# Kernel tuning notes

Hardware: AMD Instinct MI355X
Metric: run time of the kernel (lower is better)

The kernel has to match this reference:

```python
import jax, jax.numpy as jnp
import numpy as np

WS = 8   # window size
NH = 8   # num heads


def layernorm(x, g, b, eps=1e-5):
    m = jnp.mean(x, axis=-1, keepdims=True)
    v = jnp.var(x, axis=-1, keepdims=True)
    return (x - m) * jax.lax.rsqrt(v + eps) * g + b


def setup_inputs() -> dict:
    key = jax.random.key(0)
    ks = jax.random.split(key, 8)
    B, C, H, W = 16, 256, 64, 64
    s = 0.02
    inp = {
        "x": jax.random.normal(ks[0], (B, C, H, W), jnp.float32),
        "norm1_g": jnp.ones((C,), jnp.float32),
        "norm1_b": jnp.zeros((C,), jnp.float32),
        "qkv_w": jax.random.normal(ks[1], (3 * C, C), jnp.float32) * s,
        "qkv_b": jnp.zeros((3 * C,), jnp.float32),
        "rel_bias_table": jax.random.normal(ks[2], ((2 * WS - 1) ** 2, NH), jnp.float32) * s,
        "proj_w": jax.random.normal(ks[3], (C, C), jnp.float32) * s,
        "proj_b": jnp.zeros((C,), jnp.float32),
        "norm2_g": jnp.ones((C,), jnp.float32),
        "norm2_b": jnp.zeros((C,), jnp.float32),
        "fc1_w": jax.random.normal(ks[4], (4 * C, C), jnp.float32) * s,
        "fc1_b": jnp.zeros((4 * C,), jnp.float32),
        "fc2_w": jax.random.normal(ks[5], (C, 4 * C), jnp.float32) * s,
        "fc2_b": jnp.zeros((C,), jnp.float32),
    }
    # relative position index (Swin standard), shape (WS*WS, WS*WS), int constant
    coords = np.stack(np.meshgrid(np.arange(WS), np.arange(WS), indexing="ij")).reshape(2, -1)
    rel = (coords[:, :, None] - coords[:, None, :]).transpose(1, 2, 0)
    rel[:, :, 0] += WS - 1
    rel[:, :, 1] += WS - 1
    rel[:, :, 0] *= 2 * WS - 1
    inp["rel_index"] = jnp.asarray(rel.sum(-1), jnp.int32)
    return inp


def reference(x, norm1_g, norm1_b, qkv_w, qkv_b, rel_bias_table, proj_w, proj_b,
              norm2_g, norm2_b, fc1_w, fc1_b, fc2_w, fc2_b, rel_index):
    B, C, H, W = x.shape
    N = WS * WS
    hd = C // NH
    scale = hd ** -0.5

    xs = jnp.transpose(x, (0, 2, 3, 1)).reshape(B, H * W, C)  # b (h w) c
    shortcut = xs

    y = layernorm(xs, norm1_g, norm1_b).reshape(B, H, W, C)
    # window partition -> (B*nW, N, C); shift_size = 0 (default), no cyclic shift / mask
    y = y.reshape(B, H // WS, WS, W // WS, WS, C).transpose(0, 1, 3, 2, 4, 5).reshape(-1, N, C)

    qkv = (y @ qkv_w.T + qkv_b).reshape(-1, N, 3, NH, hd).transpose(2, 0, 3, 1, 4)
    q, k, v = qkv[0], qkv[1], qkv[2]  # each (nW*B, NH, N, hd)

    attn = jnp.einsum("whnd,whmd->whnm", q * scale, k)
    bias = rel_bias_table[rel_index].transpose(2, 0, 1)  # (NH, N, N)
    attn = jax.nn.softmax(attn + bias[None], axis=-1)
    out = jnp.einsum("whnm,whmd->whnd", attn, v).transpose(0, 2, 1, 3).reshape(-1, N, C)
    out = out @ proj_w.T + proj_b

    # window reverse -> (B, H*W, C)
    out = out.reshape(B, H // WS, W // WS, WS, WS, C).transpose(0, 1, 3, 2, 4, 5).reshape(B, H * W, C)

    xs = shortcut + out
    h = layernorm(xs, norm2_g, norm2_b)
    h = jax.nn.gelu(h @ fc1_w.T + fc1_b, approximate=False) @ fc2_w.T + fc2_b
    xs = xs + h

    return jnp.transpose(xs.reshape(B, H, W, C), (0, 3, 1, 2))
```

## Files before the change

### kernel.cpp

```cpp
#include <hip/hip_runtime.h>

typedef unsigned short u16;
typedef __attribute__((ext_vector_type(8))) short short8;
typedef __attribute__((ext_vector_type(4))) float f32x4;

#define MFMA16(a, b, c) __builtin_amdgcn_mfma_f32_16x16x32_bf16((a), (b), (c), 0, 0, 0)

__device__ __forceinline__ u16 f2b(float f) {
  unsigned b = __float_as_uint(f);
  b += 0x7FFFu + ((b >> 16) & 1u);
  return (u16)(b >> 16);
}

__device__ __forceinline__ void gload_lds16(const void* g, void* l) {
  __builtin_amdgcn_global_load_lds((const __attribute__((address_space(1))) void*)g,
                                   (__attribute__((address_space(3))) void*)l, 16, 0, 0);
}

__device__ __forceinline__ float fast_gelu(float x) {
  const float u = x * 0.70710678118654752f;
  const float au = fabsf(u);
  float d = 1.f + 0.3275911f * au;
  float tt;
  asm("v_rcp_f32 %0, %1" : "=v"(tt) : "v"(d));
  float p = 1.061405429f * tt - 1.453152027f;
  p = p * tt + 1.421413741f;
  p = p * tt - 0.284496736f;
  p = p * tt + 0.254829592f;
  p = p * tt;
  const float e = __expf(-u * u);
  const float erf_au = 1.f - p * e;
  return 0.5f * x * (1.f + copysignf(erf_au, x));
}

__global__ __launch_bounds__(256) void f2bf_kernel(const float* __restrict__ s,
                                                   u16* __restrict__ d, int n) {
  int i = blockIdx.x * 256 + threadIdx.x;
  if (i < n) d[i] = f2b(s[i]);
}

__global__ __launch_bounds__(256) void biasfull_kernel(const float* __restrict__ tbl,
                                                       const int* __restrict__ ridx,
                                                       float* __restrict__ o) {
  int i = blockIdx.x * 256 + threadIdx.x;
  int hm = i >> 12, nm = i & 4095;
  o[i] = tbl[ridx[nm] * 8 + hm];
}

__global__ __launch_bounds__(256) void ln1_win_kernel(const float* __restrict__ x,
                                                      const float* __restrict__ g,
                                                      const float* __restrict__ b,
                                                      u16* __restrict__ y) {
  __shared__ float red[2][4][64];
  const int bh = blockIdx.x;
  const int bb = bh >> 6, h = bh & 63;
  const int w = threadIdx.x & 63, cg = threadIdx.x >> 6;
  const float* xp = x + (size_t)bb * 1048576 + (size_t)h * 64 + w;
  float vals[64];
  float s = 0.f, ss = 0.f;
#pragma unroll
  for (int j = 0; j < 64; ++j) {
    float v = xp[(size_t)(cg * 64 + j) * 4096];
    vals[j] = v;
    s += v;
    ss += v * v;
  }
  red[0][cg][w] = s;
  red[1][cg][w] = ss;
  __syncthreads();
  const float S = red[0][0][w] + red[0][1][w] + red[0][2][w] + red[0][3][w];
  const float Q = red[1][0][w] + red[1][1][w] + red[1][2][w] + red[1][3][w];
  const float m = S * (1.f / 256.f);
  const float rstd = rsqrtf(Q * (1.f / 256.f) - m * m + 1e-5f);
  const int win = bb * 64 + ((h >> 3) << 3) + (w >> 3);
  const int tok = ((h & 7) << 3) + (w & 7);
  u16* yp = y + (size_t)win * 16384 + tok * 256 + cg * 64;
#pragma unroll
  for (int jj = 0; jj < 8; ++jj) {
    short8 o;
#pragma unroll
    for (int q = 0; q < 8; ++q) {
      const int c64 = jj * 8 + q;
      const int c = cg * 64 + c64;
      o[q] = (short)f2b((vals[c64] - m) * rstd * g[c] + b[c]);
    }
    *(short8*)&yp[jj * 8] = o;
  }
}

template <int EPI>
__global__ __launch_bounds__(256) void gemm_bt(const u16* __restrict__ A,
                                               const u16* __restrict__ W,
                                               const float* __restrict__ bias,
                                               u16* __restrict__ outh,
                                               float* __restrict__ outf,
                                               const float* __restrict__ aux,
                                               const int N, const int K) {
  __shared__ __align__(16) u16 As[2][128 * 64];
  __shared__ __align__(16) u16 Bs[2][128 * 64];
  const int ntiles = N >> 7;
  const int mt = blockIdx.x / ntiles;
  const int nt = blockIdx.x - mt * ntiles;
  const int tid = threadIdx.x;
  const int wv = tid >> 6, lane = tid & 63;
  const int wr = (wv >> 1) << 6;
  const int wc = (wv & 1) << 6;
  const int lrow = lane >> 3;
  const int lkswz = (((lane & 7) ^ (lane >> 3)) << 3);
  const int lr = lane & 15, lg = lane >> 4;
  const int swz = (lr & 7) << 3;
  f32x4 acc[4][4];
#pragma unroll
  for (int mi = 0; mi < 4; ++mi)
#pragma unroll
    for (int ni = 0; ni < 4; ++ni) acc[mi][ni] = (f32x4){0.f, 0.f, 0.f, 0.f};
  const u16* Ab = A + (size_t)mt * 128 * K;
  const u16* Wb = W + (size_t)nt * 128 * K;
  const int ntk = K >> 6;

  auto STAGE = [&](int bf, int t) {
    const int kt = t << 6;
#pragma unroll
    for (int i = 0; i < 4; ++i) {
      const int rb = wv * 32 + i * 8;
      gload_lds16(Ab + (size_t)(rb + lrow) * K + kt + lkswz, &As[bf][rb * 64]);
    }
#pragma unroll
    for (int i = 0; i < 4; ++i) {
      const int rb = wv * 32 + i * 8;
      gload_lds16(Wb + (size_t)(rb + lrow) * K + kt + lkswz, &Bs[bf][rb * 64]);
    }
  };

  STAGE(0, 0);
  __syncthreads();
  int cur = 0;
  for (int t = 0; t < ntk; ++t) {
    if (t + 1 < ntk) STAGE(cur ^ 1, t + 1);
#pragma unroll
    for (int kk = 0; kk < 2; ++kk) {
      const int kq = (kk * 32 + lg * 8) ^ swz;
      short8 a[4], bq[4];
#pragma unroll
      for (int mi = 0; mi < 4; ++mi)
        a[mi] = *(const short8*)&As[cur][(wr + mi * 16 + lr) * 64 + kq];
#pragma unroll
      for (int ni = 0; ni < 4; ++ni)
        bq[ni] = *(const short8*)&Bs[cur][(wc + ni * 16 + lr) * 64 + kq];
#pragma unroll
      for (int mi = 0; mi < 4; ++mi)
#pragma unroll
        for (int ni = 0; ni < 4; ++ni) acc[mi][ni] = MFMA16(a[mi], bq[ni], acc[mi][ni]);
    }
    __syncthreads();
    cur ^= 1;
  }
  const int row0 = mt * 128 + wr + lg * 4;
  const int col0 = nt * 128 + wc + lr;

  if constexpr (EPI == 0) {
#pragma unroll
    for (int mi = 0; mi < 4; ++mi)
#pragma unroll
      for (int ni = 0; ni < 4; ++ni) {
        const int col = col0 + ni * 16;
        const int which = col >> 8, cc = col & 255;
        const int head = cc >> 5, hd = cc & 31;
        u16* dst = outh + (size_t)which * 16777216ull;
        const float scl = (which == 0) ? 0.17677669529663689f : 1.0f;
        const float bv = bias[col];
#pragma unroll
        for (int r = 0; r < 4; ++r) {
          const int row = row0 + mi * 16 + r;
          const int win = row >> 6, tk = row & 63;
          dst[(((size_t)(win * 8 + head) << 6) + tk) * 32 + hd] =
              f2b((acc[mi][ni][r] + bv) * scl);
        }
      }
  } else if constexpr (EPI == 1) {
#pragma unroll
    for (int mi = 0; mi < 4; ++mi)
#pragma unroll
      for (int ni = 0; ni < 4; ++ni) {
        const int col = col0 + ni * 16;
        const float bv = bias[col];
#pragma unroll
        for (int r = 0; r < 4; ++r) {
          const int row = row0 + mi * 16 + r;
          const int win = row >> 6, tk = row & 63;
          const int bb = win >> 6;
          const int h = (((win >> 3) & 7) << 3) + (tk >> 3);
          const int w = ((win & 7) << 3) + (tk & 7);
          float val = acc[mi][ni][r] + bv +
                      aux[(((size_t)bb * 256 + col) * 64 + h) * 64 + w];
          outf[(size_t)row * 256 + col] = val;
        }
      }
  } else if constexpr (EPI == 2) {
#pragma unroll
    for (int mi = 0; mi < 4; ++mi)
#pragma unroll
      for (int ni = 0; ni < 4; ++ni) {
        const int col = col0 + ni * 16;
        const float bv = bias[col];
#pragma unroll
        for (int r = 0; r < 4; ++r) {
          const int row = row0 + mi * 16 + r;
          outh[(size_t)row * N + col] = f2b(fast_gelu(acc[mi][ni][r] + bv));
        }
      }
  } else {
#pragma unroll
    for (int mi = 0; mi < 4; ++mi)
#pragma unroll
      for (int ni = 0; ni < 4; ++ni) {
        const int col = col0 + ni * 16;
        const float bv = bias[col];
        const int row = row0 + mi * 16;
        const int win = row >> 6, tk = row & 63;
        const int bb = win >> 6;
        const int h = (((win >> 3) & 7) << 3) + (tk >> 3);
        const int w = ((win & 7) << 3) + (tk & 7);
        f32x4 v;
#pragma unroll
        for (int r = 0; r < 4; ++r)
          v[r] = acc[mi][ni][r] + bv + aux[(size_t)(row + r) * 256 + col];
        *(f32x4*)&outf[(((size_t)bb * 256 + col) * 64 + h) * 64 + w] = v;
      }
  }
}

__global__ __launch_bounds__(64) void attn_kernel(const u16* __restrict__ qkv,
                                                  const float* __restrict__ biasf,
                                                  u16* __restrict__ aout) {
  __shared__ __align__(16) u16 qs[64 * 40];
  __shared__ __align__(16) u16 ks[64 * 40];
  __shared__ __align__(16) u16 vt[32 * 72];
  __shared__ __align__(16) u16 pp[64 * 72];
  const int wh = blockIdx.x;
  const int head = wh & 7;
  const int win = wh >> 3;
  const int lane = threadIdx.x;
  const int lr = lane & 15, lg = lane >> 4;
  const u16* qg = qkv + (size_t)wh * 2048;
  const u16* kg = qkv + 16777216ull + (size_t)wh * 2048;
  const u16* vg = qkv + 33554432ull + (size_t)wh * 2048;
#pragma unroll
  for (int i = 0; i < 4; ++i) {
    int ch = i * 64 + lane;
    int r = ch >> 2, qo = (ch & 3) * 8;
    *(short8*)&qs[r * 40 + qo] = *(const short8*)&qg[r * 32 + qo];
    *(short8*)&ks[r * 40 + qo] = *(const short8*)&kg[r * 32 + qo];
  }
  {
    short8 v0 = *(const short8*)&vg[(size_t)lane * 32];
    short8 v1 = *(const short8*)&vg[(size_t)lane * 32 + 8];
    short8 v2 = *(const short8*)&vg[(size_t)lane * 32 + 16];
    short8 v3 = *(const short8*)&vg[(size_t)lane * 32 + 24];
#pragma unroll
    for (int j = 0; j < 8; ++j) {
      vt[j * 72 + lane] = (u16)v0[j];
      vt[(8 + j) * 72 + lane] = (u16)v1[j];
      vt[(16 + j) * 72 + lane] = (u16)v2[j];
      vt[(24 + j) * 72 + lane] = (u16)v3[j];
    }
  }
  __syncthreads();
  f32x4 sf[4][4];
#pragma unroll
  for (int mi = 0; mi < 4; ++mi)
#pragma unroll
    for (int ni = 0; ni < 4; ++ni) sf[mi][ni] = (f32x4){0.f, 0.f, 0.f, 0.f};
  {
    short8 a[4], bq[4];
#pragma unroll
    for (int mi = 0; mi < 4; ++mi) a[mi] = *(const short8*)&qs[(mi * 16 + lr) * 40 + lg * 8];
#pragma unroll
    for (int ni = 0; ni < 4; ++ni) bq[ni] = *(const short8*)&ks[(ni * 16 + lr) * 40 + lg * 8];
#pragma unroll
    for (int mi = 0; mi < 4; ++mi)
#pragma unroll
      for (int ni = 0; ni < 4; ++ni) sf[mi][ni] = MFMA16(a[mi], bq[ni], sf[mi][ni]);
  }
  const float* bh = biasf + (size_t)head * 4096;
#pragma unroll
  for (int mi = 0; mi < 4; ++mi) {
#pragma unroll
    for (int r = 0; r < 4; ++r) {
      const int n = mi * 16 + lg * 4 + r;
      float v0 = sf[mi][0][r] + bh[n * 64 + lr];
      float v1 = sf[mi][1][r] + bh[n * 64 + 16 + lr];
      float v2 = sf[mi][2][r] + bh[n * 64 + 32 + lr];
      float v3 = sf[mi][3][r] + bh[n * 64 + 48 + lr];
      float mx = fmaxf(fmaxf(v0, v1), fmaxf(v2, v3));
      mx = fmaxf(mx, __shfl_xor(mx, 1));
      mx = fmaxf(mx, __shfl_xor(mx, 2));
      mx = fmaxf(mx, __shfl_xor(mx, 4));
      mx = fmaxf(mx, __shfl_xor(mx, 8));
      float e0 = __expf(v0 - mx), e1 = __expf(v1 - mx);
      float e2 = __expf(v2 - mx), e3 = __expf(v3 - mx);
      float sm = e0 + e1 + e2 + e3;
      sm += __shfl_xor(sm, 1);
      sm += __shfl_xor(sm, 2);
      sm += __shfl_xor(sm, 4);
      sm += __shfl_xor(sm, 8);
      const float inv = 1.f / sm;
      pp[n * 72 + lr] = f2b(e0 * inv);
      pp[n * 72 + 16 + lr] = f2b(e1 * inv);
      pp[n * 72 + 32 + lr] = f2b(e2 * inv);
      pp[n * 72 + 48 + lr] = f2b(e3 * inv);
    }
  }
  __syncthreads();
  f32x4 o[4][2];
#pragma unroll
  for (int mi = 0; mi < 4; ++mi)
#pragma unroll
    for (int ni = 0; ni < 2; ++ni) o[mi][ni] = (f32x4){0.f, 0.f, 0.f, 0.f};
#pragma unroll
  for (int kk = 0; kk < 2; ++kk) {
    short8 pa[4], vb[2];
#pragma unroll
    for (int mi = 0; mi < 4; ++mi)
      pa[mi] = *(const short8*)&pp[(mi * 16 + lr) * 72 + kk * 32 + lg * 8];
#pragma unroll
    for (int ni = 0; ni < 2; ++ni)
      vb[ni] = *(const short8*)&vt[(ni * 16 + lr) * 72 + kk * 32 + lg * 8];
#pragma unroll
    for (int mi = 0; mi < 4; ++mi)
#pragma unroll
      for (int ni = 0; ni < 2; ++ni) o[mi][ni] = MFMA16(pa[mi], vb[ni], o[mi][ni]);
  }
  u16* op = aout + (size_t)win * 16384 + head * 32;
#pragma unroll
  for (int mi = 0; mi < 4; ++mi)
#pragma unroll
    for (int ni = 0; ni < 2; ++ni)
#pragma unroll
      for (int r = 0; r < 4; ++r) {
        const int n = mi * 16 + lg * 4 + r;
        op[(size_t)n * 256 + ni * 16 + lr] = f2b(o[mi][ni][r]);
      }
}

__global__ __launch_bounds__(256) void ln2_kernel(const float* __restrict__ xs2,
                                                  const float* __restrict__ g,
                                                  const float* __restrict__ b,
                                                  u16* __restrict__ h2) {
  const int wv = threadIdx.x >> 6, lane = threadIdx.x & 63;
  const size_t row = (size_t)blockIdx.x * 4 + wv;
  const f32x4 xv = *(const f32x4*)&xs2[row * 256 + lane * 4];
  float s = xv[0] + xv[1] + xv[2] + xv[3];
  float q = xv[0] * xv[0] + xv[1] * xv[1] + xv[2] * xv[2] + xv[3] * xv[3];
#pragma unroll
  for (int off = 1; off < 64; off <<= 1) {
    s += __shfl_xor(s, off);
    q += __shfl_xor(q, off);
  }
  const float m = s * (1.f / 256.f);
  const float rstd = rsqrtf(q * (1.f / 256.f) - m * m + 1e-5f);
  const f32x4 gv = *(const f32x4*)&g[lane * 4];
  const f32x4 bv = *(const f32x4*)&b[lane * 4];
  union {
    u16 u[4];
    unsigned long long v;
  } pk;
#pragma unroll
  for (int j = 0; j < 4; ++j) pk.u[j] = f2b((xv[j] - m) * rstd * gv[j] + bv[j]);
  *(unsigned long long*)&h2[row * 256 + lane * 4] = pk.v;
}

extern "C" void kernel_launch(void* const* d_in, const int* in_sizes, int n_in,
                              void* d_out, int out_size, void* d_ws, size_t ws_size,
                              hipStream_t stream) {
  const float* x = (const float*)d_in[0];
  const float* n1g = (const float*)d_in[1];
  const float* n1b = (const float*)d_in[2];
  const float* qkv_w = (const float*)d_in[3];
  const float* qkv_b = (const float*)d_in[4];
  const float* tbl = (const float*)d_in[5];
  const float* proj_w = (const float*)d_in[6];
  const float* proj_b = (const float*)d_in[7];
  const float* n2g = (const float*)d_in[8];
  const float* n2b = (const float*)d_in[9];
  const float* fc1_w = (const float*)d_in[10];
  const float* fc1_b = (const float*)d_in[11];
  const float* fc2_w = (const float*)d_in[12];
  const float* fc2_b = (const float*)d_in[13];
  const int* relidx = (const int*)d_in[14];
  float* outp = (float*)d_out;

  char* w = (char*)d_ws;
  const size_t Mi = 1ull << 20;
  if (ws_size < 237 * Mi) return;
  u16* Y = (u16*)(w + 0);
  u16* qb = (u16*)(w + 32 * Mi);
  u16* aout = (u16*)(w + 0);
  float* xs2 = (float*)(w + 32 * Mi);
  u16* h2 = (u16*)(w + 0);
  u16* h1 = (u16*)(w + 96 * Mi);
  u16* wqkv = (u16*)(w + 224 * Mi);
  u16* wproj = wqkv + 196608;
  u16* wfc1 = wproj + 65536;
  u16* wfc2 = wfc1 + 262144;
  float* bfull = (float*)(w + 224 * Mi + 1572864);

  f2bf_kernel<<<768, 256, 0, stream>>>(qkv_w, wqkv, 196608);
  f2bf_kernel<<<256, 256, 0, stream>>>(proj_w, wproj, 65536);
  f2bf_kernel<<<1024, 256, 0, stream>>>(fc1_w, wfc1, 262144);
  f2bf_kernel<<<1024, 256, 0, stream>>>(fc2_w, wfc2, 262144);
  biasfull_kernel<<<128, 256, 0, stream>>>(tbl, relidx, bfull);

  ln1_win_kernel<<<1024, 256, 0, stream>>>(x, n1g, n1b, Y);
  gemm_bt<0><<<512 * 6, 256, 0, stream>>>(Y, wqkv, qkv_b, qb, nullptr, nullptr, 768, 256);
  attn_kernel<<<8192, 64, 0, stream>>>(qb, bfull, aout);
  gemm_bt<1><<<512 * 2, 256, 0, stream>>>(aout, wproj, proj_b, nullptr, xs2, x, 256, 256);
  ln2_kernel<<<16384, 256, 0, stream>>>(xs2, n2g, n2b, h2);
  gemm_bt<2><<<512 * 8, 256, 0, stream>>>(h2, wfc1, fc1_b, h1, nullptr, nullptr, 1024, 256);
  gemm_bt<3><<<512 * 2, 256, 0, stream>>>(h1, wfc2, fc2_b, nullptr, outp, xs2, 256, 1024);
}
```

Before: 373.7 us.

## Keep weight tile in registers across M-chunks with triple-buffered A pipeline

Replaces the generic double-buffered GEMM for the K=256 GEMMs (qkv, proj, fc1) with a persistent-style kernel. Each block loads its 64-column weight slice into registers once, then loops over several 128-row A tiles through a three-stage LDS ring with explicit vmcnt waits and raw barriers, so epilogue stores overlap the next tile's loads. fc2 gets a specialised kernel with a two-deep prefetch and explicit waitcnt. The cost is heavy register pressure from the resident weight fragments and hand-counted vmcnt values that are fragile if the load counts change.

```diff
diff --git a/kernel.cpp b/kernel.cpp
--- a/kernel.cpp
+++ b/kernel.cpp
@@ -5,6 +5,9 @@
 typedef __attribute__((ext_vector_type(4))) float f32x4;
 
 #define MFMA16(a, b, c) __builtin_amdgcn_mfma_f32_16x16x32_bf16((a), (b), (c), 0, 0, 0)
+#define WAITV(N) asm volatile("s_waitcnt vmcnt(" #N ")" ::: "memory")
+#define BARS() __builtin_amdgcn_s_barrier()
+#define MFENCE() asm volatile("" ::: "memory")
 
 __device__ __forceinline__ u16 f2b(float f) {
   unsigned b = __float_as_uint(f);
@@ -88,25 +91,182 @@
   }
 }
 
-template <int EPI>
-__global__ __launch_bounds__(256) void gemm_bt(const u16* __restrict__ A,
-                                               const u16* __restrict__ W,
-                                               const float* __restrict__ bias,
-                                               u16* __restrict__ outh,
-                                               float* __restrict__ outf,
-                                               const float* __restrict__ aux,
-                                               const int N, const int K) {
+template <int EPI, int NNT, int CHUNK, int NCOLS>
+__global__ __launch_bounds__(256, 3) void gemm_pers(const u16* __restrict__ A,
+                                                    const u16* __restrict__ W,
+                                                    const float* __restrict__ bias,
+                                                    u16* __restrict__ outh,
+                                                    float* __restrict__ outf,
+                                                    const float* __restrict__ aux) {
+  __shared__ __align__(16) u16 As[3 * 8192];
+  const int bid = blockIdx.x;
+  const int nt = bid % NNT, mg = bid / NNT;
+  const int tid = threadIdx.x;
+  const int wv = tid >> 6, lane = tid & 63;
+  const int wr = (wv >> 1) << 6;
+  const int wc = (wv & 1) << 5;
+  const int lrow = lane >> 3;
+  const int lkswz = (((lane & 7) ^ lrow) << 3);
+  const int lr = lane & 15, lg = lane >> 4;
+  const int swz = (lr & 7) << 3;
+  const u16* Wb = W + (size_t)nt * 64 * 256;
+
+  {
+    const int srh = lane >> 5;
+    const int klin = (lane & 31) << 3;
+#pragma unroll
+    for (int i = 0; i < 8; ++i) {
+      const int rb2 = (i * 4 + wv) * 2;
+      const int srow = rb2 + srh;
+      gload_lds16(Wb + (size_t)srow * 256 + (klin ^ ((srow & 7) << 3)), &As[rb2 * 256]);
+    }
+  }
+  const int mt0 = mg * CHUNK * 128;
+#define STAGEA(MR, KC, RG)                                                              \
+  {                                                                                     \
+    _Pragma("unroll") for (int i_ = 0; i_ < 4; ++i_) {                                  \
+      const int rb_ = wv * 32 + i_ * 8;                                                 \
+      gload_lds16(A + (size_t)((MR) + rb_ + lrow) * 256 + (KC) * 64 + lkswz,            \
+                  &As[(RG)*8192 + rb_ * 64]);                                           \
+    }                                                                                   \
+  }
+  STAGEA(mt0, 0, 2);
+  WAITV(4);
+  BARS();
+  MFENCE();
+  short8 breg[2][8];
+#pragma unroll
+  for (int ni = 0; ni < 2; ++ni)
+#pragma unroll
+    for (int s = 0; s < 8; ++s)
+      breg[ni][s] = *(const short8*)&As[(wc + ni * 16 + lr) * 256 + ((s * 32 + lg * 8) ^ swz)];
+  asm volatile("s_waitcnt lgkmcnt(0)" ::: "memory");
+  BARS();
+  STAGEA(mt0, 1, 0);
+  STAGEA(mt0, 2, 1);
+
+  f32x4 acc[4][2];
+#pragma unroll
+  for (int mi = 0; mi < 4; ++mi)
+#pragma unroll
+    for (int ni = 0; ni < 2; ++ni) acc[mi][ni] = (f32x4){0.f, 0.f, 0.f, 0.f};
+
+#define COMPUTE(RG, KC)                                                                 \
+  {                                                                                     \
+    const u16* Ar = &As[(RG)*8192];                                                     \
+    _Pragma("unroll") for (int kk = 0; kk < 2; ++kk) {                                  \
+      const int kq = (kk * 32 + lg * 8) ^ swz;                                          \
+      short8 af[4];                                                                     \
+      _Pragma("unroll") for (int mi = 0; mi < 4; ++mi)                                  \
+          af[mi] = *(const short8*)&Ar[(wr + mi * 16 + lr) * 64 + kq];                  \
+      _Pragma("unroll") for (int mi = 0; mi < 4; ++mi)                                  \
+          _Pragma("unroll") for (int ni = 0; ni < 2; ++ni)                              \
+              acc[mi][ni] = MFMA16(af[mi], breg[ni][(KC)*2 + kk], acc[mi][ni]);         \
+    }                                                                                   \
+  }
+
+  auto EPILOG = [&](int mrow0) {
+#pragma unroll
+    for (int ni = 0; ni < 2; ++ni) {
+      const int col = nt * 64 + wc + ni * 16 + lr;
+      const float bv = bias[col];
+      if constexpr (EPI == 0) {
+        const int which = col >> 8, cc = col & 255;
+        u16* dst = outh + (size_t)which * 16777216ull + (cc & 31) + ((cc >> 5) << 11);
+        const float scl = (which == 0) ? 0.17677669529663689f : 1.0f;
+#pragma unroll
+        for (int mi = 0; mi < 4; ++mi)
+#pragma unroll
+          for (int r = 0; r < 4; ++r) {
+            const int row = mrow0 + wr + mi * 16 + lg * 4 + r;
+            const int win = row >> 6, tk = row & 63;
+            dst[(size_t)win * 16384 + (tk << 5)] = f2b((acc[mi][ni][r] + bv) * scl);
+          }
+      } else if constexpr (EPI == 1) {
+#pragma unroll
+        for (int mi = 0; mi < 4; ++mi) {
+          const int row0 = mrow0 + wr + mi * 16 + lg * 4;
+          const int win = row0 >> 6, tk = row0 & 63;
+          const int bb = win >> 6;
+          const int h = (((win >> 3) & 7) << 3) + (tk >> 3);
+          const int w0 = ((win & 7) << 3) + (tk & 7);
+          const f32x4 xv = *(const f32x4*)&aux[(((size_t)bb * 256 + col) * 64 + h) * 64 + w0];
+#pragma unroll
+          for (int r = 0; r < 4; ++r)
+            outf[(size_t)(row0 + r) * 256 + col] = acc[mi][ni][r] + bv + xv[r];
+        }
+      } else {
+#pragma unroll
+        for (int mi = 0; mi < 4; ++mi)
+#pragma unroll
+          for (int r = 0; r < 4; ++r) {
+            const int row = mrow0 + wr + mi * 16 + lg * 4 + r;
+            outh[(size_t)row * NCOLS + col] = f2b(fast_gelu(acc[mi][ni][r] + bv));
+          }
+      }
+    }
+#pragma unroll
+    for (int mi = 0; mi < 4; ++mi)
+#pragma unroll
+      for (int ni = 0; ni < 2; ++ni) acc[mi][ni] = (f32x4){0.f, 0.f, 0.f, 0.f};
+  };
+
+#define WAITV_EPI()                                  \
+  if constexpr (EPI == 1) WAITV(48); else WAITV(40)
+#define WAITV_TL2()                                  \
+  if constexpr (EPI == 1) WAITV(44); else WAITV(36)
+
+  WAITV(8); BARS(); MFENCE(); COMPUTE(2, 0); BARS(); STAGEA(mt0, 3, 2);
+  WAITV(8); BARS(); MFENCE(); COMPUTE(0, 1); BARS(); STAGEA(mt0 + 128, 0, 0);
+  WAITV(8); BARS(); MFENCE(); COMPUTE(1, 2); BARS(); STAGEA(mt0 + 128, 1, 1);
+  WAITV(8); BARS(); MFENCE(); COMPUTE(2, 3); BARS(); STAGEA(mt0 + 128, 2, 2);
+  EPILOG(mt0);
+  int rr = 0;
+  for (int m = 1; m < CHUNK - 1; ++m) {
+    const int mr = mt0 + m * 128;
+    WAITV_EPI(); BARS(); MFENCE(); COMPUTE(rr, 0); BARS(); STAGEA(mr, 3, rr);
+    rr = (rr == 2) ? 0 : rr + 1;
+    WAITV_EPI(); BARS(); MFENCE(); COMPUTE(rr, 1); BARS(); STAGEA(mr + 128, 0, rr);
+    rr = (rr == 2) ? 0 : rr + 1;
+    WAITV_EPI(); BARS(); MFENCE(); COMPUTE(rr, 2); BARS(); STAGEA(mr + 128, 1, rr);
+    rr = (rr == 2) ? 0 : rr + 1;
+    WAITV(8);   BARS(); MFENCE(); COMPUTE(rr, 3); BARS(); STAGEA(mr + 128, 2, rr);
+    rr = (rr == 2) ? 0 : rr + 1;
+    EPILOG(mr);
+  }
+  {
+    const int mr = mt0 + (CHUNK - 1) * 128;
+    WAITV_EPI(); BARS(); MFENCE(); COMPUTE(rr, 0); BARS(); STAGEA(mr, 3, rr);
+    rr = (rr == 2) ? 0 : rr + 1;
+    WAITV_EPI(); BARS(); MFENCE(); COMPUTE(rr, 1); BARS();
+    rr = (rr == 2) ? 0 : rr + 1;
+    WAITV_TL2(); BARS(); MFENCE(); COMPUTE(rr, 2); BARS();
+    rr = (rr == 2) ? 0 : rr + 1;
+    WAITV(0);    BARS(); MFENCE(); COMPUTE(rr, 3);
+    EPILOG(mr);
+  }
+#undef STAGEA
+#undef COMPUTE
+#undef WAITV_EPI
+#undef WAITV_TL2
+}
+
+__global__ __launch_bounds__(256) void gemm_fc2(const u16* __restrict__ A,
+                                                const u16* __restrict__ W,
+                                                const float* __restrict__ bias,
+                                                float* __restrict__ outf,
+                                                const float* __restrict__ aux) {
   __shared__ __align__(16) u16 As[2][128 * 64];
   __shared__ __align__(16) u16 Bs[2][128 * 64];
-  const int ntiles = N >> 7;
-  const int mt = blockIdx.x / ntiles;
-  const int nt = blockIdx.x - mt * ntiles;
+  const int K = 1024;
+  const int mt = blockIdx.x >> 1;
+  const int nt = blockIdx.x & 1;
   const int tid = threadIdx.x;
   const int wv = tid >> 6, lane = tid & 63;
   const int wr = (wv >> 1) << 6;
   const int wc = (wv & 1) << 6;
   const int lrow = lane >> 3;
-  const int lkswz = (((lane & 7) ^ (lane >> 3)) << 3);
+  const int lkswz = (((lane & 7) ^ lrow) << 3);
   const int lr = lane & 15, lg = lane >> 4;
   const int swz = (lr & 7) << 3;
   f32x4 acc[4][4];
@@ -116,118 +276,68 @@
     for (int ni = 0; ni < 4; ++ni) acc[mi][ni] = (f32x4){0.f, 0.f, 0.f, 0.f};
   const u16* Ab = A + (size_t)mt * 128 * K;
   const u16* Wb = W + (size_t)nt * 128 * K;
-  const int ntk = K >> 6;
-
-  auto STAGE = [&](int bf, int t) {
-    const int kt = t << 6;
-#pragma unroll
-    for (int i = 0; i < 4; ++i) {
-      const int rb = wv * 32 + i * 8;
-      gload_lds16(Ab + (size_t)(rb + lrow) * K + kt + lkswz, &As[bf][rb * 64]);
-    }
-#pragma unroll
-    for (int i = 0; i < 4; ++i) {
-      const int rb = wv * 32 + i * 8;
-      gload_lds16(Wb + (size_t)(rb + lrow) * K + kt + lkswz, &Bs[bf][rb * 64]);
-    }
-  };
-
-  STAGE(0, 0);
-  __syncthreads();
-  int cur = 0;
-  for (int t = 0; t < ntk; ++t) {
-    if (t + 1 < ntk) STAGE(cur ^ 1, t + 1);
-#pragma unroll
-    for (int kk = 0; kk < 2; ++kk) {
-      const int kq = (kk * 32 + lg * 8) ^ swz;
-      short8 a[4], bq[4];
-#pragma unroll
-      for (int mi = 0; mi < 4; ++mi)
-        a[mi] = *(const short8*)&As[cur][(wr + mi * 16 + lr) * 64 + kq];
-#pragma unroll
-      for (int ni = 0; ni < 4; ++ni)
-        bq[ni] = *(const short8*)&Bs[cur][(wc + ni * 16 + lr) * 64 + kq];
-#pragma unroll
-      for (int mi = 0; mi < 4; ++mi)
-#pragma unroll
-        for (int ni = 0; ni < 4; ++ni) acc[mi][ni] = MFMA16(a[mi], bq[ni], acc[mi][ni]);
-    }
-    __syncthreads();
-    cur ^= 1;
-  }
+
+#define STG(BF, T)                                                                      \
+  {                                                                                     \
+    const int kt_ = (T) << 6;                                                           \
+    _Pragma("unroll") for (int i_ = 0; i_ < 4; ++i_) {                                  \
+      const int rb_ = wv * 32 + i_ * 8;                                                 \
+      gload_lds16(Ab + (size_t)(rb_ + lrow) * K + kt_ + lkswz, &As[BF][rb_ * 64]);      \
+    }                                                                                   \
+    _Pragma("unroll") for (int i_ = 0; i_ < 4; ++i_) {                                  \
+      const int rb_ = wv * 32 + i_ * 8;                                                 \
+      gload_lds16(Wb + (size_t)(rb_ + lrow) * K + kt_ + lkswz, &Bs[BF][rb_ * 64]);      \
+    }                                                                                   \
+  }
+#define CMP(BF)                                                                         \
+  {                                                                                     \
+    _Pragma("unroll") for (int kk = 0; kk < 2; ++kk) {                                  \
+      const int kq = (kk * 32 + lg * 8) ^ swz;                                          \
+      short8 a_[4], b_[4];                                                              \
+      _Pragma("unroll") for (int mi = 0; mi < 4; ++mi)                                  \
+          a_[mi] = *(const short8*)&As[BF][(wr + mi * 16 + lr) * 64 + kq];              \
+      _Pragma("unroll") for (int ni = 0; ni < 4; ++ni)                                  \
+          b_[ni] = *(const short8*)&Bs[BF][(wc + ni * 16 + lr) * 64 + kq];              \
+      _Pragma("unroll") for (int mi = 0; mi < 4; ++mi)                                  \
+          _Pragma("unroll") for (int ni = 0; ni < 4; ++ni)                              \
+              acc[mi][ni] = MFMA16(a_[mi], b_[ni], acc[mi][ni]);                        \
+    }                                                                                   \
+  }
+  STG(0, 0);
+  STG(1, 1);
+  for (int t = 0; t < 15; ++t) {
+    WAITV(8);
+    BARS();
+    MFENCE();
+    CMP(t & 1);
+    BARS();
+    if (t + 2 < 16) STG(t & 1, t + 2);
+  }
+  WAITV(0);
+  BARS();
+  MFENCE();
+  CMP(1);
+#undef STG
+#undef CMP
   const int row0 = mt * 128 + wr + lg * 4;
   const int col0 = nt * 128 + wc + lr;
-
-  if constexpr (EPI == 0) {
-#pragma unroll
-    for (int mi = 0; mi < 4; ++mi)
-#pragma unroll
-      for (int ni = 0; ni < 4; ++ni) {
-        const int col = col0 + ni * 16;
-        const int which = col >> 8, cc = col & 255;
-        const int head = cc >> 5, hd = cc & 31;
-        u16* dst = outh + (size_t)which * 16777216ull;
-        const float scl = (which == 0) ? 0.17677669529663689f : 1.0f;
-        const float bv = bias[col];
-#pragma unroll
-        for (int r = 0; r < 4; ++r) {
-          const int row = row0 + mi * 16 + r;
-          const int win = row >> 6, tk = row & 63;
-          dst[(((size_t)(win * 8 + head) << 6) + tk) * 32 + hd] =
-              f2b((acc[mi][ni][r] + bv) * scl);
-        }
-      }
-  } else if constexpr (EPI == 1) {
-#pragma unroll
-    for (int mi = 0; mi < 4; ++mi)
-#pragma unroll
-      for (int ni = 0; ni < 4; ++ni) {
-        const int col = col0 + ni * 16;
-        const float bv = bias[col];
-#pragma unroll
-        for (int r = 0; r < 4; ++r) {
-          const int row = row0 + mi * 16 + r;
-          const int win = row >> 6, tk = row & 63;
-          const int bb = win >> 6;
-          const int h = (((win >> 3) & 7) << 3) + (tk >> 3);
-          const int w = ((win & 7) << 3) + (tk & 7);
-          float val = acc[mi][ni][r] + bv +
-                      aux[(((size_t)bb * 256 + col) * 64 + h) * 64 + w];
-          outf[(size_t)row * 256 + col] = val;
-        }
-      }
-  } else if constexpr (EPI == 2) {
-#pragma unroll
-    for (int mi = 0; mi < 4; ++mi)
-#pragma unroll
-      for (int ni = 0; ni < 4; ++ni) {
-        const int col = col0 + ni * 16;
-        const float bv = bias[col];
-#pragma unroll
-        for (int r = 0; r < 4; ++r) {
-          const int row = row0 + mi * 16 + r;
-          outh[(size_t)row * N + col] = f2b(fast_gelu(acc[mi][ni][r] + bv));
-        }
-      }
-  } else {
-#pragma unroll
-    for (int mi = 0; mi < 4; ++mi)
-#pragma unroll
-      for (int ni = 0; ni < 4; ++ni) {
-        const int col = col0 + ni * 16;
-        const float bv = bias[col];
-        const int row = row0 + mi * 16;
-        const int win = row >> 6, tk = row & 63;
-        const int bb = win >> 6;
-        const int h = (((win >> 3) & 7) << 3) + (tk >> 3);
-        const int w = ((win & 7) << 3) + (tk & 7);
-        f32x4 v;
-#pragma unroll
-        for (int r = 0; r < 4; ++r)
-          v[r] = acc[mi][ni][r] + bv + aux[(size_t)(row + r) * 256 + col];
-        *(f32x4*)&outf[(((size_t)bb * 256 + col) * 64 + h) * 64 + w] = v;
-      }
-  }
+#pragma unroll
+  for (int mi = 0; mi < 4; ++mi)
+#pragma unroll
+    for (int ni = 0; ni < 4; ++ni) {
+      const int col = col0 + ni * 16;
+      const float bv = bias[col];
+      const int row = row0 + mi * 16;
+      const int win = row >> 6, tk = row & 63;
+      const int bb = win >> 6;
+      const int h = (((win >> 3) & 7) << 3) + (tk >> 3);
+      const int w = ((win & 7) << 3) + (tk & 7);
+      f32x4 v;
+#pragma unroll
+      for (int r = 0; r < 4; ++r)
+        v[r] = acc[mi][ni][r] + bv + aux[(size_t)(row + r) * 256 + col];
+      *(f32x4*)&outf[(((size_t)bb * 256 + col) * 64 + h) * 64 + w] = v;
+    }
 }
 
 __global__ __launch_bounds__(64) void attn_kernel(const u16* __restrict__ qkv,
@@ -412,10 +522,10 @@
   biasfull_kernel<<<128, 256, 0, stream>>>(tbl, relidx, bfull);
 
   ln1_win_kernel<<<1024, 256, 0, stream>>>(x, n1g, n1b, Y);
-  gemm_bt<0><<<512 * 6, 256, 0, stream>>>(Y, wqkv, qkv_b, qb, nullptr, nullptr, 768, 256);
+  gemm_pers<0, 12, 8, 768><<<768, 256, 0, stream>>>(Y, wqkv, qkv_b, qb, nullptr, nullptr);
   attn_kernel<<<8192, 64, 0, stream>>>(qb, bfull, aout);
-  gemm_bt<1><<<512 * 2, 256, 0, stream>>>(aout, wproj, proj_b, nullptr, xs2, x, 256, 256);
+  gemm_pers<1, 4, 4, 256><<<512, 256, 0, stream>>>(aout, wproj, proj_b, nullptr, xs2, x);
   ln2_kernel<<<16384, 256, 0, stream>>>(xs2, n2g, n2b, h2);
-  gemm_bt<2><<<512 * 8, 256, 0, stream>>>(h2, wfc1, fc1_b, h1, nullptr, nullptr, 1024, 256);
-  gemm_bt<3><<<512 * 2, 256, 0, stream>>>(h1, wfc2, fc2_b, nullptr, outp, xs2, 256, 1024);
-}
+  gemm_pers<2, 16, 8, 1024><<<1024, 256, 0, stream>>>(h2, wfc1, fc1_b, h1, nullptr, nullptr);
+  gemm_fc2<<<1024, 256, 0, stream>>>(h1, wfc2, fc2_b, outp, xs2);
+}
```

New measurement: 400.7 us. +7.2%, slower.
